# Performance work log

Measured on AMD Instinct MI355X. Metric: run time of the kernel, lower is better.

## Reference

```python
import jax, jax.numpy as jnp
import numpy as np

NUM_HEADS = 32
NUM_KV_HEADS = 8
HEAD_DIM = 128
ROPE_THETA = 10000.0


def rotate_half(x):
    x1, x2 = jnp.split(x, 2, axis=-1)
    return jnp.concatenate((-x2, x1), axis=-1)


def setup_inputs() -> dict:
    key = jax.random.key(0)
    ks = jax.random.split(key, 5)
    B, S, H = 1, 2048, 4096
    KV = NUM_KV_HEADS * HEAD_DIM
    return {
        "hidden_states": jax.random.normal(ks[0], (B, S, H), dtype=jnp.float32),
        "position_ids": jnp.arange(S, dtype=jnp.int64 if jax.config.jax_enable_x64 else jnp.int32)[None, :].repeat(B, axis=0),
        "Wq": jax.random.normal(ks[1], (H, H), dtype=jnp.float32) * 0.02,
        "Wk": jax.random.normal(ks[2], (KV, H), dtype=jnp.float32) * 0.02,
        "Wv": jax.random.normal(ks[3], (KV, H), dtype=jnp.float32) * 0.02,
        "Wo": jax.random.normal(ks[4], (H, H), dtype=jnp.float32) * 0.02,
    }


def reference(hidden_states, position_ids, Wq, Wk, Wv, Wo):
    B, S, H = hidden_states.shape
    nh, nkv, hd = NUM_HEADS, NUM_KV_HEADS, HEAD_DIM
    n_rep = nh // nkv

    # QKV projections (torch Linear: y = x @ W^T)
    q = jnp.einsum('bsh,oh->bso', hidden_states, Wq).reshape(B, S, nh, hd).transpose(0, 2, 1, 3)
    k = jnp.einsum('bsh,oh->bso', hidden_states, Wk).reshape(B, S, nkv, hd).transpose(0, 2, 1, 3)
    v = jnp.einsum('bsh,oh->bso', hidden_states, Wv).reshape(B, S, nkv, hd).transpose(0, 2, 1, 3)

    # RoPE: cos/sin [B, 1, S, hd]
    inv_freq = 1.0 / (ROPE_THETA ** (jnp.arange(0, hd, 2, dtype=jnp.float32) / hd))
    freqs = position_ids.astype(jnp.float32)[..., None] * inv_freq  # [B, S, hd/2]
    emb = jnp.concatenate((freqs, freqs), axis=-1)                  # [B, S, hd]
    cos = jnp.cos(emb)[:, None, :, :]
    sin = jnp.sin(emb)[:, None, :, :]
    q = q * cos + rotate_half(q) * sin
    k = k * cos + rotate_half(k) * sin

    # GQA repeat_kv: [B, nkv, S, hd] -> [B, nh, S, hd]
    k = jnp.repeat(k, n_rep, axis=1)
    v = jnp.repeat(v, n_rep, axis=1)

    # eager attention with causal mask, softmax in fp32
    scores = jnp.einsum('bhqd,bhkd->bhqk', q, k) / jnp.sqrt(jnp.float32(hd))
    causal = jnp.tril(jnp.ones((S, S), dtype=bool))
    scores = jnp.where(causal[None, None], scores, jnp.finfo(scores.dtype).min)
    probs = jax.nn.softmax(scores.astype(jnp.float32), axis=-1).astype(q.dtype)
    attn = jnp.einsum('bhqk,bhkd->bhqd', probs, v)

    out = attn.transpose(0, 2, 1, 3).reshape(B, S, nh * hd)
    return jnp.einsum('bso,ho->bsh', out, Wo)
```

## Files before the change

### kernel.cpp

```cpp
#include <hip/hip_runtime.h>

typedef __bf16 bf16x8 __attribute__((ext_vector_type(8)));
typedef float f32x4 __attribute__((ext_vector_type(4)));
typedef unsigned int u32x4 __attribute__((ext_vector_type(4)));
typedef unsigned short u16x4 __attribute__((ext_vector_type(4)));
typedef unsigned short ushort_t;

#define S_LEN 2048
#define HDIM  4096
#define KVDIM 1024
#define NHEAD 32
#define NKV   8

__device__ __forceinline__ unsigned short f2b(float x) {
    unsigned int u = __builtin_bit_cast(unsigned int, x);
    u = (u + 0x7FFFu + ((u >> 16) & 1u)) >> 16;
    return (unsigned short)u;
}
__device__ __forceinline__ float b2f(unsigned short b) {
    unsigned int u = ((unsigned int)b) << 16;
    return __builtin_bit_cast(float, u);
}

__device__ __forceinline__ void gl_lds16(const void* g, void* s) {
    __builtin_amdgcn_global_load_lds(
        (const __attribute__((address_space(1))) unsigned int*)g,
        (__attribute__((address_space(3))) unsigned int*)s, 16, 0, 0);
}

__global__ void cvt_kernel(const float* __restrict__ in, unsigned short* __restrict__ out, int n4) {
    int i = blockIdx.x * 256 + threadIdx.x;
    if (i >= n4) return;
    f32x4 v = ((const f32x4*)in)[i];
    u16x4 o;
    o.x = f2b(v.x); o.y = f2b(v.y); o.z = f2b(v.z); o.w = f2b(v.w);
    ((u16x4*)out)[i] = o;
}

template <int MODE>
__device__ __forceinline__ void gemm_body(const unsigned short* __restrict__ A,
                                          const unsigned short* __restrict__ B,
                                          void* __restrict__ Cv,
                                          int M, int N, int K, int m0, int n0,
                                          unsigned short (*As)[64], unsigned short (*Bs)[64]) {
    const int tid = threadIdx.x;
    const int w = tid >> 6, lane = tid & 63, quad = lane >> 4, l15 = lane & 15;
    const int wy = w >> 1, wx = w & 1;
    const int srowb = w * 32 + (lane >> 3);
    const int gchunk = (lane & 7) ^ (lane >> 3);
    const int lcol = (lane & 7) * 8;

    f32x4 acc[4][4] = {};

    for (int k0 = 0; k0 < K; k0 += 64) {
#pragma unroll
        for (int p = 0; p < 4; ++p) {
            int r = srowb + p * 8;
            gl_lds16(&A[(size_t)(m0 + r) * K + k0 + gchunk * 8], &As[r][lcol]);
            gl_lds16(&B[(size_t)(n0 + r) * K + k0 + gchunk * 8], &Bs[r][lcol]);
        }
        __syncthreads();
#pragma unroll
        for (int t = 0; t < 2; ++t) {
            bf16x8 af[4], bfr[4];
#pragma unroll
            for (int mb = 0; mb < 4; ++mb)
                af[mb] = *(const bf16x8*)&As[wy * 64 + mb * 16 + l15][(((t * 4 + quad) ^ (l15 & 7)) * 8)];
#pragma unroll
            for (int nb = 0; nb < 4; ++nb)
                bfr[nb] = *(const bf16x8*)&Bs[wx * 64 + nb * 16 + l15][(((t * 4 + quad) ^ (l15 & 7)) * 8)];
#pragma unroll
            for (int mb = 0; mb < 4; ++mb)
#pragma unroll
                for (int nb = 0; nb < 4; ++nb)
                    acc[mb][nb] = __builtin_amdgcn_mfma_f32_16x16x32_bf16(af[mb], bfr[nb], acc[mb][nb], 0, 0, 0);
        }
        __syncthreads();
    }
#pragma unroll
    for (int mb = 0; mb < 4; ++mb)
#pragma unroll
        for (int nb = 0; nb < 4; ++nb)
#pragma unroll
            for (int r = 0; r < 4; ++r) {
                int row = m0 + wy * 64 + mb * 16 + quad * 4 + r;
                int col = n0 + wx * 64 + nb * 16 + l15;
                float v = acc[mb][nb][r];
                if (MODE == 0)
                    ((unsigned short*)Cv)[(size_t)row * N + col] = f2b(v);
                else if (MODE == 1)
                    ((unsigned short*)Cv)[(size_t)col * M + row] = f2b(v);
                else
                    ((float*)Cv)[(size_t)row * N + col] = v;
            }
}

template <int MODE>
__global__ __launch_bounds__(256) void gemm_nt(const unsigned short* __restrict__ A,
                                               const unsigned short* __restrict__ B,
                                               void* __restrict__ Cv, int M, int N, int K) {
    __shared__ unsigned short As[128][64];
    __shared__ unsigned short Bs[128][64];
    gemm_body<MODE>(A, B, Cv, M, N, K, blockIdx.y * 128, blockIdx.x * 128, As, Bs);
}

__global__ __launch_bounds__(256) void gemm_kv(const unsigned short* __restrict__ A,
                                               const unsigned short* __restrict__ Bk,
                                               const unsigned short* __restrict__ Bv,
                                               void* __restrict__ Ck, void* __restrict__ Cvt,
                                               int M, int K) {
    __shared__ unsigned short As[128][64];
    __shared__ unsigned short Bs[128][64];
    if (blockIdx.x < 8)
        gemm_body<0>(A, Bk, Ck, M, KVDIM, K, blockIdx.y * 128, blockIdx.x * 128, As, Bs);
    else
        gemm_body<1>(A, Bv, Cvt, M, KVDIM, K, blockIdx.y * 128, (blockIdx.x - 8) * 128, As, Bs);
}

__global__ void rope_kernel(unsigned short* __restrict__ Q, unsigned short* __restrict__ Kc,
                            const int* __restrict__ pos_ids) {
    int tid = blockIdx.x * 256 + threadIdx.x;
    int j = tid & 63;
    int head = (tid >> 6) % (NHEAD + NKV);
    int s = tid / (64 * (NHEAD + NKV));
    float pos = (float)pos_ids[s];
    float inv = exp2f(-(float)j * 0.20762050593046f);
    float ang = pos * inv;
    float sn, cs;
    __sincosf(ang, &sn, &cs);
    unsigned short* p;
    if (head < NHEAD)
        p = Q + (size_t)s * HDIM + head * 128;
    else
        p = Kc + (size_t)s * KVDIM + (head - NHEAD) * 128;
    float x1 = b2f(p[j]), x2 = b2f(p[j + 64]);
    p[j] = f2b(x1 * cs - x2 * sn);
    p[j + 64] = f2b(x2 * cs + x1 * sn);
}

__global__ __launch_bounds__(256) void attn_fwd(const unsigned short* __restrict__ Q,
                                                const unsigned short* __restrict__ Kb,
                                                const unsigned short* __restrict__ Vt,
                                                unsigned short* __restrict__ O) {
    __shared__ unsigned short Ks[64][136];
    __shared__ unsigned short Vts[128][72];
    __shared__ unsigned short Ps[4][16][80];

    const int qblk = (gridDim.y - 1) - blockIdx.y;
    const int h = blockIdx.x, kvh = h >> 2;
    const int tid = threadIdx.x, w = tid >> 6, lane = tid & 63;
    const int quad = lane >> 4, l15 = lane & 15;
    const int qg = qblk * 64 + w * 16 + l15;

    bf16x8 aq[4];
#pragma unroll
    for (int t = 0; t < 4; ++t)
        aq[t] = *(const bf16x8*)&Q[(size_t)qg * HDIM + h * 128 + t * 32 + quad * 8];

    f32x4 o[8] = {};
    float m_s = -3.0e38f, l_s = 0.f;
    const float cexp = 0.08838834764831845f * 1.4426950408889634f;

    const int kr0 = tid >> 4, ksg = tid & 15;
    const int vr0 = tid >> 3, vsg = tid & 7;

    u32x4 kpre[4], vpre[4];
#pragma unroll
    for (int p = 0; p < 4; ++p) {
        kpre[p] = *(const u32x4*)&Kb[(size_t)(kr0 + p * 16) * KVDIM + kvh * 128 + ksg * 8];
        vpre[p] = *(const u32x4*)&Vt[(size_t)(kvh * 128 + vr0 + p * 32) * S_LEN + vsg * 8];
    }

    for (int kt = 0; kt <= qblk; ++kt) {
#pragma unroll
        for (int p = 0; p < 4; ++p) {
            *(u32x4*)&Ks[kr0 + p * 16][ksg * 8] = kpre[p];
            *(u32x4*)&Vts[vr0 + p * 32][vsg * 8] = vpre[p];
        }
        __syncthreads();
        if (kt < qblk) {
            const int k0n = kt * 64 + 64;
#pragma unroll
            for (int p = 0; p < 4; ++p) {
                kpre[p] = *(const u32x4*)&Kb[(size_t)(k0n + kr0 + p * 16) * KVDIM + kvh * 128 + ksg * 8];
                vpre[p] = *(const u32x4*)&Vt[(size_t)(kvh * 128 + vr0 + p * 32) * S_LEN + k0n + vsg * 8];
            }
        }

        f32x4 sc[4] = {};
#pragma unroll
        for (int t = 0; t < 4; ++t)
#pragma unroll
            for (int mb = 0; mb < 4; ++mb) {
                bf16x8 ak = *(const bf16x8*)&Ks[mb * 16 + l15][t * 32 + quad * 8];
                sc[mb] = __builtin_amdgcn_mfma_f32_16x16x32_bf16(ak, aq[t], sc[mb], 0, 0, 0);
            }

        float vv[16];
        if (kt == qblk) {
#pragma unroll
            for (int mb = 0; mb < 4; ++mb)
#pragma unroll
                for (int r = 0; r < 4; ++r) {
                    int kl = mb * 16 + quad * 4 + r;
                    vv[mb * 4 + r] = (kl <= w * 16 + l15) ? sc[mb][r] * cexp : -3.0e38f;
                }
        } else {
#pragma unroll
            for (int mb = 0; mb < 4; ++mb)
#pragma unroll
                for (int r = 0; r < 4; ++r)
                    vv[mb * 4 + r] = sc[mb][r] * cexp;
        }
        float mx = vv[0];
#pragma unroll
        for (int i = 1; i < 16; ++i) mx = fmaxf(mx, vv[i]);
        mx = fmaxf(mx, __shfl_xor(mx, 16, 64));
        mx = fmaxf(mx, __shfl_xor(mx, 32, 64));
        float mnew = fmaxf(m_s, mx);
        float alpha = exp2f(m_s - mnew);
        m_s = mnew;
        float sum = 0.f;
        unsigned short pb[16];
#pragma unroll
        for (int i = 0; i < 16; ++i) {
            float pp = exp2f(vv[i] - mnew);
            sum += pp;
            pb[i] = f2b(pp);
        }
        sum += __shfl_xor(sum, 16, 64);
        sum += __shfl_xor(sum, 32, 64);
        l_s = l_s * alpha + sum;
#pragma unroll
        for (int mb = 0; mb < 4; ++mb) {
            u16x4 pk = {pb[mb * 4 + 0], pb[mb * 4 + 1], pb[mb * 4 + 2], pb[mb * 4 + 3]};
            *(u16x4*)&Ps[w][l15][mb * 16 + quad * 4] = pk;
        }
        float a4[4];
#pragma unroll
        for (int r = 0; r < 4; ++r) a4[r] = __shfl(alpha, quad * 20 + r, 64);
#pragma unroll
        for (int db = 0; db < 8; ++db)
#pragma unroll
            for (int r = 0; r < 4; ++r) o[db][r] *= a4[r];

        bf16x8 pa[2];
#pragma unroll
        for (int t = 0; t < 2; ++t)
            pa[t] = *(const bf16x8*)&Ps[w][l15][t * 32 + quad * 8];
#pragma unroll
        for (int db = 0; db < 8; ++db)
#pragma unroll
            for (int t = 0; t < 2; ++t) {
                bf16x8 vb = *(const bf16x8*)&Vts[db * 16 + l15][t * 32 + quad * 8];
                o[db] = __builtin_amdgcn_mfma_f32_16x16x32_bf16(pa[t], vb, o[db], 0, 0, 0);
            }
        __syncthreads();
    }

    float linv[4];
#pragma unroll
    for (int r = 0; r < 4; ++r) linv[r] = 1.0f / __shfl(l_s, quad * 20 + r, 64);
    const int qrow_base = qblk * 64 + w * 16 + quad * 4;
#pragma unroll
    for (int db = 0; db < 8; ++db)
#pragma unroll
        for (int r = 0; r < 4; ++r) {
            int row = qrow_base + r;
            int col = h * 128 + db * 16 + l15;
            O[(size_t)row * HDIM + col] = f2b(o[db][r] * linv[r]);
        }
}

extern "C" void kernel_launch(void* const* d_in, const int* in_sizes, int n_in,
                              void* d_out, int out_size, void* d_ws, size_t ws_size,
                              hipStream_t stream) {
    const float* hid = (const float*)d_in[0];
    const int* pos   = (const int*)d_in[1];
    const float* Wq  = (const float*)d_in[2];
    const float* Wk  = (const float*)d_in[3];
    const float* Wv  = (const float*)d_in[4];
    const float* Wo  = (const float*)d_in[5];
    float* out = (float*)d_out;

    char* ws = (char*)d_ws;
    unsigned short* hb   = (unsigned short*)(ws);
    unsigned short* Wqb  = (unsigned short*)(ws + 16777216);
    unsigned short* Wkb  = (unsigned short*)(ws + 50331648);
    unsigned short* Wvb  = (unsigned short*)(ws + 58720256);
    unsigned short* Wob  = (unsigned short*)(ws + 67108864);
    unsigned short* Qw   = (unsigned short*)(ws + 100663296);
    unsigned short* Kw   = (unsigned short*)(ws + 117440512);
    unsigned short* Vtw  = Wqb;
    unsigned short* attw = hb;

    cvt_kernel<<<(S_LEN * HDIM / 4 + 255) / 256, 256, 0, stream>>>(hid, hb, S_LEN * HDIM / 4);
    cvt_kernel<<<(HDIM * HDIM / 4 + 255) / 256, 256, 0, stream>>>(Wq, Wqb, HDIM * HDIM / 4);
    cvt_kernel<<<(KVDIM * HDIM / 4 + 255) / 256, 256, 0, stream>>>(Wk, Wkb, KVDIM * HDIM / 4);
    cvt_kernel<<<(KVDIM * HDIM / 4 + 255) / 256, 256, 0, stream>>>(Wv, Wvb, KVDIM * HDIM / 4);
    cvt_kernel<<<(HDIM * HDIM / 4 + 255) / 256, 256, 0, stream>>>(Wo, Wob, HDIM * HDIM / 4);

    gemm_nt<0><<<dim3(HDIM / 128, S_LEN / 128), 256, 0, stream>>>(hb, Wqb, Qw, S_LEN, HDIM, HDIM);
    gemm_kv<<<dim3(16, S_LEN / 128), 256, 0, stream>>>(hb, Wkb, Wvb, Kw, Vtw, S_LEN, HDIM);

    rope_kernel<<<S_LEN * (NHEAD + NKV) * 64 / 256, 256, 0, stream>>>(Qw, Kw, pos);

    attn_fwd<<<dim3(NHEAD, S_LEN / 64), 256, 0, stream>>>(Qw, Kw, Vtw, attw);

    gemm_nt<2><<<dim3(HDIM / 128, S_LEN / 128), 256, 0, stream>>>(attw, Wob, out, S_LEN, HDIM, HDIM);
}
```

Measured before the change: 556.2 us.

## Replace 128x128 GEMMs with pipelined 256x256 double-buffered GEMM and fuse QKV

Replaces the simple 128x128 single-buffered GEMM with a 256x256-tile, 512-thread kernel. It double-buffers LDS, issues async global-to-LDS loads two K-steps ahead, splits each step into four MFMA quadrants separated by barriers, and raises wave priority around the MFMA blocks. The Q, K and V projections are fused into one GEMM over a concatenated 6144-wide weight, with an epilogue that routes outputs to Q, K and transposed V. The aim is to hide memory latency behind MFMA work, improve data reuse, and cut launch count. In exchange it uses more LDS and registers, and the grid gets smaller (192 and 128 blocks), which may underfill the CUs.

```diff
diff --git a/kernel.cpp b/kernel.cpp
--- a/kernel.cpp
+++ b/kernel.cpp
@@ -4,13 +4,15 @@
 typedef float f32x4 __attribute__((ext_vector_type(4)));
 typedef unsigned int u32x4 __attribute__((ext_vector_type(4)));
 typedef unsigned short u16x4 __attribute__((ext_vector_type(4)));
-typedef unsigned short ushort_t;
 
 #define S_LEN 2048
 #define HDIM  4096
 #define KVDIM 1024
 #define NHEAD 32
 #define NKV   8
+#define QKVN  6144
+#define GK    4096
+#define GNT   (GK / 64)
 
 __device__ __forceinline__ unsigned short f2b(float x) {
     unsigned int u = __builtin_bit_cast(unsigned int, x);
@@ -27,6 +29,14 @@
         (const __attribute__((address_space(1))) unsigned int*)g,
         (__attribute__((address_space(3))) unsigned int*)s, 16, 0, 0);
 }
+
+__device__ __forceinline__ void sbar() {
+    asm volatile("" ::: "memory");
+    __builtin_amdgcn_s_barrier();
+    asm volatile("" ::: "memory");
+    __builtin_amdgcn_sched_barrier(0);
+}
+#define WAITVM(n) asm volatile("s_waitcnt vmcnt(" #n ")" ::: "memory")
 
 __global__ void cvt_kernel(const float* __restrict__ in, unsigned short* __restrict__ out, int n4) {
     int i = blockIdx.x * 256 + threadIdx.x;
@@ -38,83 +48,148 @@
 }
 
 template <int MODE>
-__device__ __forceinline__ void gemm_body(const unsigned short* __restrict__ A,
-                                          const unsigned short* __restrict__ B,
-                                          void* __restrict__ Cv,
-                                          int M, int N, int K, int m0, int n0,
-                                          unsigned short (*As)[64], unsigned short (*Bs)[64]) {
+__global__ __launch_bounds__(512, 2) void gemm256(const unsigned short* __restrict__ A,
+                                                  const unsigned short* __restrict__ B,
+                                                  void* __restrict__ C0,
+                                                  unsigned short* __restrict__ C1,
+                                                  unsigned short* __restrict__ C2,
+                                                  int N) {
+    __shared__ unsigned short Am[2][2][128][64];
+    __shared__ unsigned short Bn[2][2][128][64];
+
     const int tid = threadIdx.x;
-    const int w = tid >> 6, lane = tid & 63, quad = lane >> 4, l15 = lane & 15;
-    const int wy = w >> 1, wx = w & 1;
-    const int srowb = w * 32 + (lane >> 3);
-    const int gchunk = (lane & 7) ^ (lane >> 3);
-    const int lcol = (lane & 7) * 8;
-
-    f32x4 acc[4][4] = {};
-
-    for (int k0 = 0; k0 < K; k0 += 64) {
-#pragma unroll
-        for (int p = 0; p < 4; ++p) {
-            int r = srowb + p * 8;
-            gl_lds16(&A[(size_t)(m0 + r) * K + k0 + gchunk * 8], &As[r][lcol]);
-            gl_lds16(&B[(size_t)(n0 + r) * K + k0 + gchunk * 8], &Bs[r][lcol]);
-        }
-        __syncthreads();
-#pragma unroll
-        for (int t = 0; t < 2; ++t) {
-            bf16x8 af[4], bfr[4];
-#pragma unroll
-            for (int mb = 0; mb < 4; ++mb)
-                af[mb] = *(const bf16x8*)&As[wy * 64 + mb * 16 + l15][(((t * 4 + quad) ^ (l15 & 7)) * 8)];
-#pragma unroll
-            for (int nb = 0; nb < 4; ++nb)
-                bfr[nb] = *(const bf16x8*)&Bs[wx * 64 + nb * 16 + l15][(((t * 4 + quad) ^ (l15 & 7)) * 8)];
-#pragma unroll
-            for (int mb = 0; mb < 4; ++mb)
-#pragma unroll
-                for (int nb = 0; nb < 4; ++nb)
-                    acc[mb][nb] = __builtin_amdgcn_mfma_f32_16x16x32_bf16(af[mb], bfr[nb], acc[mb][nb], 0, 0, 0);
-        }
-        __syncthreads();
+    const int w = tid >> 6, lane = tid & 63;
+    const int quad = lane >> 4, l15 = lane & 15;
+    const int wy = w >> 2, wx = w & 3;
+    const int rsub = lane >> 3, csl = lane & 7;
+    const int gch = csl ^ rsub;
+    const int m0 = blockIdx.y * 256, n0 = blockIdx.x * 256;
+
+    f32x4 acc[8][4] = {};
+
+    auto stageA = [&](int mh, int par, int kt) {
+        if (kt < GNT) {
+#pragma unroll
+            for (int i = 0; i < 2; ++i) {
+                int grow = m0 + i * 128 + mh * 64 + w * 8 + rsub;
+                gl_lds16(&A[(size_t)grow * GK + kt * 64 + gch * 8],
+                         &Am[mh][par][i * 64 + w * 8 + rsub][csl * 8]);
+            }
+        }
+    };
+    auto stageB = [&](int nh, int par, int kt) {
+        if (kt < GNT) {
+#pragma unroll
+            for (int i = 0; i < 2; ++i) {
+                int lr = i * 64 + w * 8 + rsub;
+                int gn = n0 + (lr >> 5) * 64 + nh * 32 + (lr & 31);
+                gl_lds16(&B[(size_t)gn * GK + kt * 64 + gch * 8],
+                         &Bn[nh][par][lr][csl * 8]);
+            }
+        }
+    };
+    auto rdA = [&](int mh, int par, int mbl, int t) -> bf16x8 {
+        return *(const bf16x8*)&Am[mh][par][wy * 64 + mbl * 16 + l15][(((t * 4 + quad) ^ (l15 & 7)) * 8)];
+    };
+    auto rdB = [&](int nh, int par, int nbl, int t) -> bf16x8 {
+        return *(const bf16x8*)&Bn[nh][par][wx * 32 + nbl * 16 + l15][(((t * 4 + quad) ^ (l15 & 7)) * 8)];
+    };
+
+    stageA(0, 0, 0); stageB(0, 0, 0); stageB(1, 0, 0); stageA(1, 0, 0);
+    stageA(0, 1, 1); stageB(1, 1, 1); stageA(1, 1, 1);
+    WAITVM(6);
+    sbar();
+
+    for (int j = 0; j < GNT; ++j) {
+        const int par = j & 1, parn = par ^ 1;
+        bf16x8 a[4][2], b[2][2];
+
+#pragma unroll
+        for (int mb = 0; mb < 4; ++mb) { a[mb][0] = rdA(0, par, mb, 0); a[mb][1] = rdA(0, par, mb, 1); }
+#pragma unroll
+        for (int nb = 0; nb < 2; ++nb) { b[nb][0] = rdB(0, par, nb, 0); b[nb][1] = rdB(0, par, nb, 1); }
+        stageB(0, parn, j + 1);
+        sbar();
+        __builtin_amdgcn_s_setprio(1);
+#pragma unroll
+        for (int mb = 0; mb < 4; ++mb)
+#pragma unroll
+            for (int nb = 0; nb < 2; ++nb) {
+                acc[mb][nb] = __builtin_amdgcn_mfma_f32_16x16x32_bf16(a[mb][0], b[nb][0], acc[mb][nb], 0, 0, 0);
+                acc[mb][nb] = __builtin_amdgcn_mfma_f32_16x16x32_bf16(a[mb][1], b[nb][1], acc[mb][nb], 0, 0, 0);
+            }
+        __builtin_amdgcn_s_setprio(0);
+        sbar();
+
+#pragma unroll
+        for (int nb = 0; nb < 2; ++nb) { b[nb][0] = rdB(1, par, nb, 0); b[nb][1] = rdB(1, par, nb, 1); }
+        stageA(0, par, j + 2);
+        sbar();
+        __builtin_amdgcn_s_setprio(1);
+#pragma unroll
+        for (int mb = 0; mb < 4; ++mb)
+#pragma unroll
+            for (int nb = 0; nb < 2; ++nb) {
+                acc[mb][nb + 2] = __builtin_amdgcn_mfma_f32_16x16x32_bf16(a[mb][0], b[nb][0], acc[mb][nb + 2], 0, 0, 0);
+                acc[mb][nb + 2] = __builtin_amdgcn_mfma_f32_16x16x32_bf16(a[mb][1], b[nb][1], acc[mb][nb + 2], 0, 0, 0);
+            }
+        __builtin_amdgcn_s_setprio(0);
+        sbar();
+
+#pragma unroll
+        for (int mb = 0; mb < 4; ++mb) { a[mb][0] = rdA(1, par, mb, 0); a[mb][1] = rdA(1, par, mb, 1); }
+        stageB(1, par, j + 2);
+        sbar();
+        __builtin_amdgcn_s_setprio(1);
+#pragma unroll
+        for (int mb = 0; mb < 4; ++mb)
+#pragma unroll
+            for (int nb = 0; nb < 2; ++nb) {
+                acc[mb + 4][nb + 2] = __builtin_amdgcn_mfma_f32_16x16x32_bf16(a[mb][0], b[nb][0], acc[mb + 4][nb + 2], 0, 0, 0);
+                acc[mb + 4][nb + 2] = __builtin_amdgcn_mfma_f32_16x16x32_bf16(a[mb][1], b[nb][1], acc[mb + 4][nb + 2], 0, 0, 0);
+            }
+        __builtin_amdgcn_s_setprio(0);
+        sbar();
+
+#pragma unroll
+        for (int nb = 0; nb < 2; ++nb) { b[nb][0] = rdB(0, par, nb, 0); b[nb][1] = rdB(0, par, nb, 1); }
+        stageA(1, par, j + 2);
+        sbar();
+        __builtin_amdgcn_s_setprio(1);
+#pragma unroll
+        for (int mb = 0; mb < 4; ++mb)
+#pragma unroll
+            for (int nb = 0; nb < 2; ++nb) {
+                acc[mb + 4][nb] = __builtin_amdgcn_mfma_f32_16x16x32_bf16(a[mb][0], b[nb][0], acc[mb + 4][nb], 0, 0, 0);
+                acc[mb + 4][nb] = __builtin_amdgcn_mfma_f32_16x16x32_bf16(a[mb][1], b[nb][1], acc[mb + 4][nb], 0, 0, 0);
+            }
+        __builtin_amdgcn_s_setprio(0);
+        if (j + 2 < GNT) { WAITVM(6); } else { WAITVM(0); }
+        sbar();
     }
-#pragma unroll
-    for (int mb = 0; mb < 4; ++mb)
+
+#pragma unroll
+    for (int mb = 0; mb < 8; ++mb)
 #pragma unroll
         for (int nb = 0; nb < 4; ++nb)
 #pragma unroll
             for (int r = 0; r < 4; ++r) {
-                int row = m0 + wy * 64 + mb * 16 + quad * 4 + r;
-                int col = n0 + wx * 64 + nb * 16 + l15;
+                int row = m0 + wy * 128 + mb * 16 + quad * 4 + r;
+                int gc = n0 + wx * 64 + nb * 16 + l15;
                 float v = acc[mb][nb][r];
-                if (MODE == 0)
-                    ((unsigned short*)Cv)[(size_t)row * N + col] = f2b(v);
-                else if (MODE == 1)
-                    ((unsigned short*)Cv)[(size_t)col * M + row] = f2b(v);
-                else
-                    ((float*)Cv)[(size_t)row * N + col] = v;
-            }
-}
-
-template <int MODE>
-__global__ __launch_bounds__(256) void gemm_nt(const unsigned short* __restrict__ A,
-                                               const unsigned short* __restrict__ B,
-                                               void* __restrict__ Cv, int M, int N, int K) {
-    __shared__ unsigned short As[128][64];
-    __shared__ unsigned short Bs[128][64];
-    gemm_body<MODE>(A, B, Cv, M, N, K, blockIdx.y * 128, blockIdx.x * 128, As, Bs);
-}
-
-__global__ __launch_bounds__(256) void gemm_kv(const unsigned short* __restrict__ A,
-                                               const unsigned short* __restrict__ Bk,
-                                               const unsigned short* __restrict__ Bv,
-                                               void* __restrict__ Ck, void* __restrict__ Cvt,
-                                               int M, int K) {
-    __shared__ unsigned short As[128][64];
-    __shared__ unsigned short Bs[128][64];
-    if (blockIdx.x < 8)
-        gemm_body<0>(A, Bk, Ck, M, KVDIM, K, blockIdx.y * 128, blockIdx.x * 128, As, Bs);
-    else
-        gemm_body<1>(A, Bv, Cvt, M, KVDIM, K, blockIdx.y * 128, (blockIdx.x - 8) * 128, As, Bs);
+                if (MODE == 0) {
+                    ((unsigned short*)C0)[(size_t)row * N + gc] = f2b(v);
+                } else if (MODE == 1) {
+                    ((float*)C0)[(size_t)row * N + gc] = v;
+                } else {
+                    if (gc < HDIM)
+                        ((unsigned short*)C0)[(size_t)row * HDIM + gc] = f2b(v);
+                    else if (gc < HDIM + KVDIM)
+                        C1[(size_t)row * KVDIM + (gc - HDIM)] = f2b(v);
+                    else
+                        C2[(size_t)(gc - HDIM - KVDIM) * S_LEN + row] = f2b(v);
+                }
+            }
 }
 
 __global__ void rope_kernel(unsigned short* __restrict__ Q, unsigned short* __restrict__ Kc,
@@ -284,28 +359,26 @@
     float* out = (float*)d_out;
 
     char* ws = (char*)d_ws;
-    unsigned short* hb   = (unsigned short*)(ws);
-    unsigned short* Wqb  = (unsigned short*)(ws + 16777216);
-    unsigned short* Wkb  = (unsigned short*)(ws + 50331648);
-    unsigned short* Wvb  = (unsigned short*)(ws + 58720256);
-    unsigned short* Wob  = (unsigned short*)(ws + 67108864);
-    unsigned short* Qw   = (unsigned short*)(ws + 100663296);
-    unsigned short* Kw   = (unsigned short*)(ws + 117440512);
-    unsigned short* Vtw  = Wqb;
-    unsigned short* attw = hb;
+    unsigned short* hb    = (unsigned short*)(ws);
+    unsigned short* Wqkvb = (unsigned short*)(ws + (16ull << 20));
+    unsigned short* Wob   = (unsigned short*)(ws + (16ull << 20));
+    unsigned short* Qw    = (unsigned short*)(ws + (64ull << 20));
+    unsigned short* Kw    = (unsigned short*)(ws + (80ull << 20));
+    unsigned short* Vtw   = (unsigned short*)(ws + (84ull << 20));
+    unsigned short* attw  = hb;
 
     cvt_kernel<<<(S_LEN * HDIM / 4 + 255) / 256, 256, 0, stream>>>(hid, hb, S_LEN * HDIM / 4);
-    cvt_kernel<<<(HDIM * HDIM / 4 + 255) / 256, 256, 0, stream>>>(Wq, Wqb, HDIM * HDIM / 4);
-    cvt_kernel<<<(KVDIM * HDIM / 4 + 255) / 256, 256, 0, stream>>>(Wk, Wkb, KVDIM * HDIM / 4);
-    cvt_kernel<<<(KVDIM * HDIM / 4 + 255) / 256, 256, 0, stream>>>(Wv, Wvb, KVDIM * HDIM / 4);
+    cvt_kernel<<<(HDIM * HDIM / 4 + 255) / 256, 256, 0, stream>>>(Wq, Wqkvb, HDIM * HDIM / 4);
+    cvt_kernel<<<(KVDIM * HDIM / 4 + 255) / 256, 256, 0, stream>>>(Wk, Wqkvb + (size_t)HDIM * HDIM, KVDIM * HDIM / 4);
+    cvt_kernel<<<(KVDIM * HDIM / 4 + 255) / 256, 256, 0, stream>>>(Wv, Wqkvb + (size_t)(HDIM + KVDIM) * HDIM, KVDIM * HDIM / 4);
+
+    gemm256<2><<<dim3(QKVN / 256, S_LEN / 256), 512, 0, stream>>>(hb, Wqkvb, Qw, Kw, Vtw, QKVN);
+
     cvt_kernel<<<(HDIM * HDIM / 4 + 255) / 256, 256, 0, stream>>>(Wo, Wob, HDIM * HDIM / 4);
 
-    gemm_nt<0><<<dim3(HDIM / 128, S_LEN / 128), 256, 0, stream>>>(hb, Wqb, Qw, S_LEN, HDIM, HDIM);
-    gemm_kv<<<dim3(16, S_LEN / 128), 256, 0, stream>>>(hb, Wkb, Wvb, Kw, Vtw, S_LEN, HDIM);
-
     rope_kernel<<<S_LEN * (NHEAD + NKV) * 64 / 256, 256, 0, stream>>>(Qw, Kw, pos);
 
     attn_fwd<<<dim3(NHEAD, S_LEN / 64), 256, 0, stream>>>(Qw, Kw, Vtw, attw);
 
-    gemm_nt<2><<<dim3(HDIM / 128, S_LEN / 128), 256, 0, stream>>>(attw, Wob, out, S_LEN, HDIM, HDIM);
-}
+    gemm256<1><<<dim3(HDIM / 256, S_LEN / 256), 512, 0, stream>>>(attw, Wob, out, nullptr, nullptr, HDIM);
+}
```

New measurement: 575.9 us. 1.04x slower.
